# Performance work log

Hardware: AMD Instinct MI355X
Metric: run time of the kernel (lower is better)

Reference implementation:

```python
import jax, jax.numpy as jnp
import numpy as np

# DeepSeek-V3 MoE config (matches init_kwargs)
H = 1024          # hidden_size
I = 704           # moe_intermediate_size
E = 64            # n_routed_experts
TOP_K = 8         # num_experts_per_tok
NG = 8            # n_group
TOPK_GROUP = 4    # topk_group
N_SHARED = 2      # n_shared_experts
ROUTED_SCALE = 2.5
S_I = I * N_SHARED  # shared expert intermediate size


def setup_inputs() -> dict:
    key = jax.random.key(0)
    ks = jax.random.split(key, 10)
    sc = 0.02
    return {
        "hidden_states": jax.random.normal(ks[0], (1, 1024, H), dtype=jnp.float32),
        "gate_w": sc * jax.random.normal(ks[1], (E, H), dtype=jnp.float32),
        "gate_bias": sc * jax.random.normal(ks[2], (E,), dtype=jnp.float32),  # e_score_correction_bias
        "Wg": sc * jax.random.normal(ks[3], (E, I, H), dtype=jnp.float32),
        "Wu": sc * jax.random.normal(ks[4], (E, I, H), dtype=jnp.float32),
        "Wd": sc * jax.random.normal(ks[5], (E, H, I), dtype=jnp.float32),
        "Sg": sc * jax.random.normal(ks[6], (S_I, H), dtype=jnp.float32),
        "Su": sc * jax.random.normal(ks[7], (S_I, H), dtype=jnp.float32),
        "Sd": sc * jax.random.normal(ks[8], (H, S_I), dtype=jnp.float32),
    }


def _route(x, gate_w, gate_bias):
    # x: [T, H] -> dense routing weight matrix [T, E]
    T = x.shape[0]
    logits = x @ gate_w.T                         # [T, E] (fp32, as HF casts to float32)
    scores = jax.nn.sigmoid(logits)
    scores_for_choice = scores + gate_bias[None, :]
    # group scores: sum of top-2 expert scores in each group
    grp = scores_for_choice.reshape(T, NG, E // NG)
    group_scores = jnp.sum(jax.lax.top_k(grp, 2)[0], axis=-1)      # [T, NG]
    _, gidx = jax.lax.top_k(group_scores, TOPK_GROUP)              # [T, TOPK_GROUP]
    gmask = jnp.zeros((T, NG), dtype=scores.dtype).at[
        jnp.arange(T)[:, None], gidx].set(1.0)                      # [T, NG]
    emask = jnp.repeat(gmask, E // NG, axis=1)                      # [T, E]
    masked = jnp.where(emask > 0, scores_for_choice, 0.0)
    _, topk_idx = jax.lax.top_k(masked, TOP_K)                      # [T, TOP_K]
    topk_w = jnp.take_along_axis(scores, topk_idx, axis=1)          # gather from UNbiased scores
    topk_w = topk_w / (jnp.sum(topk_w, axis=-1, keepdims=True) + 1e-20)  # norm_topk_prob
    topk_w = topk_w * ROUTED_SCALE
    # dense [T, E] combine weights (zeros for unrouted experts)
    rw = jnp.zeros((T, E), dtype=scores.dtype).at[
        jnp.arange(T)[:, None], topk_idx].add(topk_w)
    return rw


def _mlp(x, gw, uw, dw):
    # SwiGLU MLP: down(silu(gate(x)) * up(x)), no biases
    return (jax.nn.silu(x @ gw.T) * (x @ uw.T)) @ dw.T


def reference(hidden_states, gate_w, gate_bias, Wg, Wu, Wd, Sg, Su, Sd):
    B, S, _ = hidden_states.shape
    x = hidden_states.reshape(B * S, H)                 # [T, H]
    rw = _route(x, gate_w, gate_bias)                   # [T, E]
    # dense reference: run every expert on every token, weighted combine
    expert_out = jax.vmap(lambda gw_, uw_, dw_: _mlp(x, gw_, uw_, dw_))(Wg, Wu, Wd)  # [E, T, H]
    routed = jnp.einsum('eth,te->th', expert_out, rw)   # [T, H]
    shared = _mlp(x, Sg, Su, Sd)                        # [T, H]
    out = (routed + shared).reshape(B, S, H)
    return out
```

## Files before the change

### kernel.cpp

```cpp
#include <hip/hip_runtime.h>
#include <hip/hip_bf16.h>
#include <cstdint>
#include <cstddef>

#define T_TOK 1024
#define H_DIM 1024
#define I_DIM 704
#define E_NUM 64
#define TOPK 8
#define NGRP 8
#define GSIZE 8
#define TOPKG 4
#define SI_DIM 1408
#define RSCALE 2.5f
#define NSLOT (T_TOK * TOPK)

#define AP 72

typedef short bf16x8 __attribute__((ext_vector_type(8)));
typedef float f32x4 __attribute__((ext_vector_type(4)));

__device__ inline unsigned pk2(float x, float y) {
    __hip_bfloat162 h2 = __float22bfloat162_rn(make_float2(x, y));
    unsigned u; __builtin_memcpy(&u, &h2, 4); return u;
}
__device__ inline unsigned short bf1(float x) {
    __hip_bfloat16 h = __float2bfloat16(x);
    unsigned short u; __builtin_memcpy(&u, &h, 2); return u;
}

__global__ __launch_bounds__(64) void route_kernel(
    const float* __restrict__ x, const float* __restrict__ gw, const float* __restrict__ gb,
    int* __restrict__ counts, int* __restrict__ tk_idx, float* __restrict__ tk_w)
{
    const int t = blockIdx.x;
    __shared__ float xs[H_DIM];
    __shared__ float raw[E_NUM];
    __shared__ float sc[E_NUM];
    __shared__ float masked[E_NUM];
    __shared__ float gsc[NGRP];
    const int tid = threadIdx.x;

    const float4* xrow = (const float4*)(x + (size_t)t * H_DIM);
    for (int i = tid; i < H_DIM / 4; i += 64) ((float4*)xs)[i] = xrow[i];
    __syncthreads();

    float a = 0.f;
    const float* w = gw + (size_t)tid * H_DIM;
    for (int h = 0; h < H_DIM; h += 4) {
        float4 w4 = *(const float4*)(w + h);
        a += xs[h] * w4.x + xs[h+1] * w4.y + xs[h+2] * w4.z + xs[h+3] * w4.w;
    }
    float s = 1.f / (1.f + expf(-a));
    raw[tid] = s;
    sc[tid] = s + gb[tid];
    __syncthreads();

    if (tid == 0) {
        for (int g = 0; g < NGRP; ++g) {
            float m1 = -1e30f, m2 = -1e30f;
            for (int j = 0; j < GSIZE; ++j) {
                float v = sc[g * GSIZE + j];
                if (v > m1) { m2 = m1; m1 = v; }
                else if (v > m2) { m2 = v; }
            }
            gsc[g] = m1 + m2;
        }
        bool gsel[NGRP];
        for (int g = 0; g < NGRP; ++g) gsel[g] = false;
        for (int k = 0; k < TOPKG; ++k) {
            int best = -1; float bv = -1e30f;
            for (int g = 0; g < NGRP; ++g)
                if (!gsel[g] && gsc[g] > bv) { bv = gsc[g]; best = g; }
            gsel[best] = true;
        }
        for (int e = 0; e < E_NUM; ++e)
            masked[e] = gsel[e / GSIZE] ? sc[e] : 0.0f;
        int idx[TOPK];
        float wsum = 0.f;
        for (int k = 0; k < TOPK; ++k) {
            int best = 0; float bv = -1e30f;
            for (int e = 0; e < E_NUM; ++e)
                if (masked[e] > bv) { bv = masked[e]; best = e; }
            masked[best] = -1e30f;
            idx[k] = best;
            wsum += raw[best];
        }
        float inv = RSCALE / (wsum + 1e-20f);
        for (int k = 0; k < TOPK; ++k) {
            tk_idx[t * TOPK + k] = idx[k];
            tk_w[t * TOPK + k] = raw[idx[k]] * inv;
            atomicAdd(&counts[idx[k]], 1);
        }
    }
}

__global__ void zero_kernel(int* counts, int* fillc)
{
    int i = threadIdx.x;
    if (i < E_NUM) { counts[i] = 0; fillc[i] = 0; }
}

__global__ void scan_kernel(const int* __restrict__ counts, int* __restrict__ offs)
{
    if (threadIdx.x == 0) {
        int acc = 0;
        for (int e = 0; e < E_NUM; ++e) { offs[e] = acc; acc += counts[e]; }
    }
}

__global__ void fill_kernel(const int* __restrict__ tk_idx, const float* __restrict__ tk_w,
                            const int* __restrict__ offs, int* __restrict__ fillc,
                            int* __restrict__ tok_list, float* __restrict__ w_list)
{
    int t = blockIdx.x * blockDim.x + threadIdx.x;
    if (t >= T_TOK) return;
    for (int k = 0; k < TOPK; ++k) {
        int e = tk_idx[t * TOPK + k];
        int pos = offs[e] + atomicAdd(&fillc[e], 1);
        tok_list[pos] = t;
        w_list[pos] = tk_w[t * TOPK + k];
    }
}

__global__ __launch_bounds__(256) void gateup_routed_mfma(
    const float* __restrict__ x, const float* __restrict__ Wg, const float* __restrict__ Wu,
    const int* __restrict__ offs, const int* __restrict__ counts,
    const int* __restrict__ tok_list, const float* __restrict__ w_list,
    unsigned short* __restrict__ act)
{
    const int e = blockIdx.z;
    const int cnt = counts[e];
    const int m0 = blockIdx.y * 128;
    if (m0 >= cnt) return;
    const int off = offs[e];
    const int n0 = blockIdx.x * 64;

    __shared__ unsigned short As[128 * AP];
    __shared__ unsigned short Bg[64 * AP];
    __shared__ unsigned short Bu[64 * AP];
    __shared__ int toks[128];
    __shared__ float wts[128];

    const int tid = threadIdx.x;
    if (tid < 128) {
        int s = m0 + tid;
        toks[tid] = (s < cnt) ? tok_list[off + s] : -1;
        wts[tid]  = (s < cnt) ? w_list[off + s] : 0.f;
    }
    __syncthreads();

    const int lane = tid & 63;
    const int wv = tid >> 6;
    const int lr = lane & 15;
    const int lq = lane >> 4;

    f32x4 accg[2][4], accu[2][4];
    #pragma unroll
    for (int i = 0; i < 2; ++i)
        #pragma unroll
        for (int j = 0; j < 4; ++j) {
            accg[i][j] = (f32x4){0.f, 0.f, 0.f, 0.f};
            accu[i][j] = (f32x4){0.f, 0.f, 0.f, 0.f};
        }

    const float* wgp = Wg + (size_t)e * I_DIM * H_DIM + (size_t)n0 * H_DIM;
    const float* wup = Wu + (size_t)e * I_DIM * H_DIM + (size_t)n0 * H_DIM;

    const int ar = tid >> 4;
    const int ac = (tid & 15) * 4;

    for (int k0 = 0; k0 < H_DIM; k0 += 64) {
        #pragma unroll
        for (int p = 0; p < 8; ++p) {
            int r = ar + p * 16;
            int tkn = toks[r];
            float4 v = make_float4(0.f, 0.f, 0.f, 0.f);
            if (tkn >= 0) v = *(const float4*)(x + (size_t)tkn * H_DIM + k0 + ac);
            *(uint2*)&As[r * AP + ac] = make_uint2(pk2(v.x, v.y), pk2(v.z, v.w));
        }
        #pragma unroll
        for (int p = 0; p < 4; ++p) {
            int r = ar + p * 16;
            float4 g = *(const float4*)(wgp + (size_t)r * H_DIM + k0 + ac);
            *(uint2*)&Bg[r * AP + ac] = make_uint2(pk2(g.x, g.y), pk2(g.z, g.w));
            float4 u = *(const float4*)(wup + (size_t)r * H_DIM + k0 + ac);
            *(uint2*)&Bu[r * AP + ac] = make_uint2(pk2(u.x, u.y), pk2(u.z, u.w));
        }
        __syncthreads();
        #pragma unroll
        for (int ks = 0; ks < 2; ++ks) {
            bf16x8 a0 = *(const bf16x8*)&As[(wv * 32 + lr) * AP + ks * 32 + lq * 8];
            bf16x8 a1 = *(const bf16x8*)&As[(wv * 32 + 16 + lr) * AP + ks * 32 + lq * 8];
            #pragma unroll
            for (int nj = 0; nj < 4; ++nj) {
                bf16x8 bg = *(const bf16x8*)&Bg[(nj * 16 + lr) * AP + ks * 32 + lq * 8];
                bf16x8 bu = *(const bf16x8*)&Bu[(nj * 16 + lr) * AP + ks * 32 + lq * 8];
                accg[0][nj] = __builtin_amdgcn_mfma_f32_16x16x32_bf16(a0, bg, accg[0][nj], 0, 0, 0);
                accg[1][nj] = __builtin_amdgcn_mfma_f32_16x16x32_bf16(a1, bg, accg[1][nj], 0, 0, 0);
                accu[0][nj] = __builtin_amdgcn_mfma_f32_16x16x32_bf16(a0, bu, accu[0][nj], 0, 0, 0);
                accu[1][nj] = __builtin_amdgcn_mfma_f32_16x16x32_bf16(a1, bu, accu[1][nj], 0, 0, 0);
            }
        }
        __syncthreads();
    }

    #pragma unroll
    for (int mi = 0; mi < 2; ++mi) {
        #pragma unroll
        for (int r = 0; r < 4; ++r) {
            int srow = wv * 32 + mi * 16 + lq * 4 + r;
            if (m0 + srow < cnt) {
                float w = wts[srow];
                unsigned short* ap = act + (size_t)(off + m0 + srow) * I_DIM + n0 + lr;
                #pragma unroll
                for (int nj = 0; nj < 4; ++nj) {
                    float g = accg[mi][nj][r];
                    float u = accu[mi][nj][r];
                    float a = w * (g / (1.f + __expf(-g))) * u;
                    ap[nj * 16] = bf1(a);
                }
            }
        }
    }
}

__global__ __launch_bounds__(256) void down_routed_mfma(
    const unsigned short* __restrict__ act, const float* __restrict__ Wd,
    const int* __restrict__ offs, const int* __restrict__ counts,
    const int* __restrict__ tok_list, float* __restrict__ out)
{
    const int e = blockIdx.z;
    const int cnt = counts[e];
    const int m0 = blockIdx.y * 128;
    if (m0 >= cnt) return;
    const int off = offs[e];
    const int n0 = blockIdx.x * 64;

    __shared__ unsigned short As[128 * AP];
    __shared__ unsigned short Bs[64 * AP];
    __shared__ int toks[128];

    const int tid = threadIdx.x;
    if (tid < 128) {
        int s = m0 + tid;
        toks[tid] = (s < cnt) ? tok_list[off + s] : 0;
    }
    __syncthreads();

    const int lane = tid & 63;
    const int wv = tid >> 6;
    const int lr = lane & 15;
    const int lq = lane >> 4;

    f32x4 acc[2][4];
    #pragma unroll
    for (int i = 0; i < 2; ++i)
        #pragma unroll
        for (int j = 0; j < 4; ++j)
            acc[i][j] = (f32x4){0.f, 0.f, 0.f, 0.f};

    const float* wdp = Wd + (size_t)e * H_DIM * I_DIM + (size_t)n0 * I_DIM;
    const unsigned short* ap0 = act + (size_t)(off + m0) * I_DIM;
    const int ar = tid >> 4;
    const int ac = (tid & 15) * 4;

    for (int k0 = 0; k0 < I_DIM; k0 += 64) {
        #pragma unroll
        for (int p = 0; p < 8; ++p) {
            int r = ar + p * 16;
            uint2 v = make_uint2(0u, 0u);
            if (m0 + r < cnt) v = *(const uint2*)(ap0 + (size_t)r * I_DIM + k0 + ac);
            *(uint2*)&As[r * AP + ac] = v;
        }
        #pragma unroll
        for (int p = 0; p < 4; ++p) {
            int r = ar + p * 16;
            float4 w4 = *(const float4*)(wdp + (size_t)r * I_DIM + k0 + ac);
            *(uint2*)&Bs[r * AP + ac] = make_uint2(pk2(w4.x, w4.y), pk2(w4.z, w4.w));
        }
        __syncthreads();
        #pragma unroll
        for (int ks = 0; ks < 2; ++ks) {
            bf16x8 a0 = *(const bf16x8*)&As[(wv * 32 + lr) * AP + ks * 32 + lq * 8];
            bf16x8 a1 = *(const bf16x8*)&As[(wv * 32 + 16 + lr) * AP + ks * 32 + lq * 8];
            #pragma unroll
            for (int nj = 0; nj < 4; ++nj) {
                bf16x8 b = *(const bf16x8*)&Bs[(nj * 16 + lr) * AP + ks * 32 + lq * 8];
                acc[0][nj] = __builtin_amdgcn_mfma_f32_16x16x32_bf16(a0, b, acc[0][nj], 0, 0, 0);
                acc[1][nj] = __builtin_amdgcn_mfma_f32_16x16x32_bf16(a1, b, acc[1][nj], 0, 0, 0);
            }
        }
        __syncthreads();
    }

    #pragma unroll
    for (int mi = 0; mi < 2; ++mi) {
        #pragma unroll
        for (int r = 0; r < 4; ++r) {
            int srow = wv * 32 + mi * 16 + lq * 4 + r;
            if (m0 + srow < cnt) {
                int t = toks[srow];
                float* op = out + (size_t)t * H_DIM + n0 + lr;
                #pragma unroll
                for (int nj = 0; nj < 4; ++nj)
                    atomicAdd(&op[nj * 16], acc[mi][nj][r]);
            }
        }
    }
}

__global__ __launch_bounds__(256) void gateup_shared_mfma(
    const float* __restrict__ x, const float* __restrict__ Sg, const float* __restrict__ Su,
    unsigned short* __restrict__ sact)
{
    const int m0 = blockIdx.y * 128;
    const int n0 = blockIdx.x * 64;

    __shared__ unsigned short As[128 * AP];
    __shared__ unsigned short Bg[64 * AP];
    __shared__ unsigned short Bu[64 * AP];

    const int tid = threadIdx.x;
    const int lane = tid & 63;
    const int wv = tid >> 6;
    const int lr = lane & 15;
    const int lq = lane >> 4;

    f32x4 accg[2][4], accu[2][4];
    #pragma unroll
    for (int i = 0; i < 2; ++i)
        #pragma unroll
        for (int j = 0; j < 4; ++j) {
            accg[i][j] = (f32x4){0.f, 0.f, 0.f, 0.f};
            accu[i][j] = (f32x4){0.f, 0.f, 0.f, 0.f};
        }

    const float* gp = Sg + (size_t)n0 * H_DIM;
    const float* up = Su + (size_t)n0 * H_DIM;
    const int ar = tid >> 4;
    const int ac = (tid & 15) * 4;

    for (int k0 = 0; k0 < H_DIM; k0 += 64) {
        #pragma unroll
        for (int p = 0; p < 8; ++p) {
            int r = ar + p * 16;
            float4 v = *(const float4*)(x + (size_t)(m0 + r) * H_DIM + k0 + ac);
            *(uint2*)&As[r * AP + ac] = make_uint2(pk2(v.x, v.y), pk2(v.z, v.w));
        }
        #pragma unroll
        for (int p = 0; p < 4; ++p) {
            int r = ar + p * 16;
            float4 g = *(const float4*)(gp + (size_t)r * H_DIM + k0 + ac);
            *(uint2*)&Bg[r * AP + ac] = make_uint2(pk2(g.x, g.y), pk2(g.z, g.w));
            float4 u = *(const float4*)(up + (size_t)r * H_DIM + k0 + ac);
            *(uint2*)&Bu[r * AP + ac] = make_uint2(pk2(u.x, u.y), pk2(u.z, u.w));
        }
        __syncthreads();
        #pragma unroll
        for (int ks = 0; ks < 2; ++ks) {
            bf16x8 a0 = *(const bf16x8*)&As[(wv * 32 + lr) * AP + ks * 32 + lq * 8];
            bf16x8 a1 = *(const bf16x8*)&As[(wv * 32 + 16 + lr) * AP + ks * 32 + lq * 8];
            #pragma unroll
            for (int nj = 0; nj < 4; ++nj) {
                bf16x8 bg = *(const bf16x8*)&Bg[(nj * 16 + lr) * AP + ks * 32 + lq * 8];
                bf16x8 bu = *(const bf16x8*)&Bu[(nj * 16 + lr) * AP + ks * 32 + lq * 8];
                accg[0][nj] = __builtin_amdgcn_mfma_f32_16x16x32_bf16(a0, bg, accg[0][nj], 0, 0, 0);
                accg[1][nj] = __builtin_amdgcn_mfma_f32_16x16x32_bf16(a1, bg, accg[1][nj], 0, 0, 0);
                accu[0][nj] = __builtin_amdgcn_mfma_f32_16x16x32_bf16(a0, bu, accu[0][nj], 0, 0, 0);
                accu[1][nj] = __builtin_amdgcn_mfma_f32_16x16x32_bf16(a1, bu, accu[1][nj], 0, 0, 0);
            }
        }
        __syncthreads();
    }

    #pragma unroll
    for (int mi = 0; mi < 2; ++mi) {
        #pragma unroll
        for (int r = 0; r < 4; ++r) {
            int trow = m0 + wv * 32 + mi * 16 + lq * 4 + r;
            unsigned short* sp = sact + (size_t)trow * SI_DIM + n0 + lr;
            #pragma unroll
            for (int nj = 0; nj < 4; ++nj) {
                float g = accg[mi][nj][r];
                float u = accu[mi][nj][r];
                float a = (g / (1.f + __expf(-g))) * u;
                sp[nj * 16] = bf1(a);
            }
        }
    }
}

__global__ __launch_bounds__(256) void down_shared_mfma(
    const unsigned short* __restrict__ sact, const float* __restrict__ Sd,
    float* __restrict__ out)
{
    const int m0 = blockIdx.y * 128;
    const int n0 = blockIdx.x * 64;

    __shared__ unsigned short As[128 * AP];
    __shared__ unsigned short Bs[64 * AP];

    const int tid = threadIdx.x;
    const int lane = tid & 63;
    const int wv = tid >> 6;
    const int lr = lane & 15;
    const int lq = lane >> 4;

    f32x4 acc[2][4];
    #pragma unroll
    for (int i = 0; i < 2; ++i)
        #pragma unroll
        for (int j = 0; j < 4; ++j)
            acc[i][j] = (f32x4){0.f, 0.f, 0.f, 0.f};

    const float* wp = Sd + (size_t)n0 * SI_DIM;
    const int ar = tid >> 4;
    const int ac = (tid & 15) * 4;

    for (int k0 = 0; k0 < SI_DIM; k0 += 64) {
        #pragma unroll
        for (int p = 0; p < 8; ++p) {
            int r = ar + p * 16;
            uint2 v = *(const uint2*)(sact + (size_t)(m0 + r) * SI_DIM + k0 + ac);
            *(uint2*)&As[r * AP + ac] = v;
        }
        #pragma unroll
        for (int p = 0; p < 4; ++p) {
            int r = ar + p * 16;
            float4 w4 = *(const float4*)(wp + (size_t)r * SI_DIM + k0 + ac);
            *(uint2*)&Bs[r * AP + ac] = make_uint2(pk2(w4.x, w4.y), pk2(w4.z, w4.w));
        }
        __syncthreads();
        #pragma unroll
        for (int ks = 0; ks < 2; ++ks) {
            bf16x8 a0 = *(const bf16x8*)&As[(wv * 32 + lr) * AP + ks * 32 + lq * 8];
            bf16x8 a1 = *(const bf16x8*)&As[(wv * 32 + 16 + lr) * AP + ks * 32 + lq * 8];
            #pragma unroll
            for (int nj = 0; nj < 4; ++nj) {
                bf16x8 b = *(const bf16x8*)&Bs[(nj * 16 + lr) * AP + ks * 32 + lq * 8];
                acc[0][nj] = __builtin_amdgcn_mfma_f32_16x16x32_bf16(a0, b, acc[0][nj], 0, 0, 0);
                acc[1][nj] = __builtin_amdgcn_mfma_f32_16x16x32_bf16(a1, b, acc[1][nj], 0, 0, 0);
            }
        }
        __syncthreads();
    }

    #pragma unroll
    for (int mi = 0; mi < 2; ++mi) {
        #pragma unroll
        for (int r = 0; r < 4; ++r) {
            int trow = m0 + wv * 32 + mi * 16 + lq * 4 + r;
            float* op = out + (size_t)trow * H_DIM + n0 + lr;
            #pragma unroll
            for (int nj = 0; nj < 4; ++nj)
                op[nj * 16] = acc[mi][nj][r];
        }
    }
}

extern "C" void kernel_launch(void* const* d_in, const int* in_sizes, int n_in,
                              void* d_out, int out_size, void* d_ws, size_t ws_size,
                              hipStream_t stream)
{
    const float* x  = (const float*)d_in[0];
    const float* gw = (const float*)d_in[1];
    const float* gb = (const float*)d_in[2];
    const float* Wg = (const float*)d_in[3];
    const float* Wu = (const float*)d_in[4];
    const float* Wd = (const float*)d_in[5];
    const float* Sg = (const float*)d_in[6];
    const float* Su = (const float*)d_in[7];
    const float* Sd = (const float*)d_in[8];
    float* out = (float*)d_out;

    unsigned short* act  = (unsigned short*)d_ws;
    unsigned short* sact = act + (size_t)NSLOT * I_DIM;
    int* counts   = (int*)(sact + (size_t)T_TOK * SI_DIM);
    int* fillc    = counts + 64;
    int* offs     = fillc + 64;
    int* tk_idx   = offs + 64;
    float* tk_w   = (float*)(tk_idx + NSLOT);
    int* tok_list = (int*)(tk_w + NSLOT);
    float* w_list = (float*)(tok_list + NSLOT);

    zero_kernel<<<1, 64, 0, stream>>>(counts, fillc);
    route_kernel<<<T_TOK, 64, 0, stream>>>(x, gw, gb, counts, tk_idx, tk_w);
    scan_kernel<<<1, 64, 0, stream>>>(counts, offs);
    fill_kernel<<<4, 256, 0, stream>>>(tk_idx, tk_w, offs, fillc, tok_list, w_list);

    gateup_routed_mfma<<<dim3(11, 8, 64), 256, 0, stream>>>(x, Wg, Wu, offs, counts, tok_list, w_list, act);
    gateup_shared_mfma<<<dim3(22, 8, 1), 256, 0, stream>>>(x, Sg, Su, sact);
    down_shared_mfma<<<dim3(16, 8, 1), 256, 0, stream>>>(sact, Sd, out);
    down_routed_mfma<<<dim3(16, 8, 64), 256, 0, stream>>>(act, Wd, offs, counts, tok_list, out);
}
```

Before: 843.7 us.

## Register-prefetch next K tile in all GEMMs and replace atomic scatter with combine kernel

Each of the four MFMA GEMM kernels now issues the global loads for the next 64-wide K tile into registers before running the MFMAs on the current LDS tile, then converts and stores them to LDS after a barrier. This hides global-load latency behind compute. The routed down projection also stops doing float atomicAdd into the output. It writes per-slot results to a new workspace buffer, and a separate combine kernel sums the eight slots per token using positions recorded by fill_kernel. This trades atomic contention for extra workspace traffic, about 32 MB of slot_out, plus one more launch. The result is also deterministic.

```diff
diff --git a/kernel.cpp b/kernel.cpp
--- a/kernel.cpp
+++ b/kernel.cpp
@@ -111,7 +111,8 @@
 
 __global__ void fill_kernel(const int* __restrict__ tk_idx, const float* __restrict__ tk_w,
                             const int* __restrict__ offs, int* __restrict__ fillc,
-                            int* __restrict__ tok_list, float* __restrict__ w_list)
+                            int* __restrict__ tok_list, float* __restrict__ w_list,
+                            int* __restrict__ tk_pos)
 {
     int t = blockIdx.x * blockDim.x + threadIdx.x;
     if (t >= T_TOK) return;
@@ -120,6 +121,7 @@
         int pos = offs[e] + atomicAdd(&fillc[e], 1);
         tok_list[pos] = t;
         w_list[pos] = tk_w[t * TOPK + k];
+        tk_pos[t * TOPK + k] = pos;
     }
 }
 
@@ -145,7 +147,7 @@
     const int tid = threadIdx.x;
     if (tid < 128) {
         int s = m0 + tid;
-        toks[tid] = (s < cnt) ? tok_list[off + s] : -1;
+        toks[tid] = (s < cnt) ? tok_list[off + s] : 0;
         wts[tid]  = (s < cnt) ? w_list[off + s] : 0.f;
     }
     __syncthreads();
@@ -154,6 +156,15 @@
     const int wv = tid >> 6;
     const int lr = lane & 15;
     const int lq = lane >> 4;
+    const int ar = tid >> 4;
+    const int ac = (tid & 15) * 4;
+
+    const float* ax[8];
+    #pragma unroll
+    for (int p = 0; p < 8; ++p)
+        ax[p] = x + (size_t)toks[ar + p * 16] * H_DIM + ac;
+    const float* wgp = Wg + (size_t)e * I_DIM * H_DIM + (size_t)(n0 + ar) * H_DIM + ac;
+    const float* wup = Wu + (size_t)e * I_DIM * H_DIM + (size_t)(n0 + ar) * H_DIM + ac;
 
     f32x4 accg[2][4], accu[2][4];
     #pragma unroll
@@ -164,30 +175,36 @@
             accu[i][j] = (f32x4){0.f, 0.f, 0.f, 0.f};
         }
 
-    const float* wgp = Wg + (size_t)e * I_DIM * H_DIM + (size_t)n0 * H_DIM;
-    const float* wup = Wu + (size_t)e * I_DIM * H_DIM + (size_t)n0 * H_DIM;
-
-    const int ar = tid >> 4;
-    const int ac = (tid & 15) * 4;
+    float4 pa[8], pbg[4], pbu[4];
+
+    #pragma unroll
+    for (int p = 0; p < 8; ++p) pa[p] = *(const float4*)(ax[p]);
+    #pragma unroll
+    for (int p = 0; p < 4; ++p) {
+        pbg[p] = *(const float4*)(wgp + (size_t)p * 16 * H_DIM);
+        pbu[p] = *(const float4*)(wup + (size_t)p * 16 * H_DIM);
+    }
+    #pragma unroll
+    for (int p = 0; p < 8; ++p)
+        *(uint2*)&As[(ar + p * 16) * AP + ac] = make_uint2(pk2(pa[p].x, pa[p].y), pk2(pa[p].z, pa[p].w));
+    #pragma unroll
+    for (int p = 0; p < 4; ++p) {
+        *(uint2*)&Bg[(ar + p * 16) * AP + ac] = make_uint2(pk2(pbg[p].x, pbg[p].y), pk2(pbg[p].z, pbg[p].w));
+        *(uint2*)&Bu[(ar + p * 16) * AP + ac] = make_uint2(pk2(pbu[p].x, pbu[p].y), pk2(pbu[p].z, pbu[p].w));
+    }
+    __syncthreads();
 
     for (int k0 = 0; k0 < H_DIM; k0 += 64) {
-        #pragma unroll
-        for (int p = 0; p < 8; ++p) {
-            int r = ar + p * 16;
-            int tkn = toks[r];
-            float4 v = make_float4(0.f, 0.f, 0.f, 0.f);
-            if (tkn >= 0) v = *(const float4*)(x + (size_t)tkn * H_DIM + k0 + ac);
-            *(uint2*)&As[r * AP + ac] = make_uint2(pk2(v.x, v.y), pk2(v.z, v.w));
-        }
-        #pragma unroll
-        for (int p = 0; p < 4; ++p) {
-            int r = ar + p * 16;
-            float4 g = *(const float4*)(wgp + (size_t)r * H_DIM + k0 + ac);
-            *(uint2*)&Bg[r * AP + ac] = make_uint2(pk2(g.x, g.y), pk2(g.z, g.w));
-            float4 u = *(const float4*)(wup + (size_t)r * H_DIM + k0 + ac);
-            *(uint2*)&Bu[r * AP + ac] = make_uint2(pk2(u.x, u.y), pk2(u.z, u.w));
-        }
-        __syncthreads();
+        const int kn = k0 + 64;
+        if (kn < H_DIM) {
+            #pragma unroll
+            for (int p = 0; p < 8; ++p) pa[p] = *(const float4*)(ax[p] + kn);
+            #pragma unroll
+            for (int p = 0; p < 4; ++p) {
+                pbg[p] = *(const float4*)(wgp + (size_t)p * 16 * H_DIM + kn);
+                pbu[p] = *(const float4*)(wup + (size_t)p * 16 * H_DIM + kn);
+            }
+        }
         #pragma unroll
         for (int ks = 0; ks < 2; ++ks) {
             bf16x8 a0 = *(const bf16x8*)&As[(wv * 32 + lr) * AP + ks * 32 + lq * 8];
@@ -201,6 +218,16 @@
                 accu[0][nj] = __builtin_amdgcn_mfma_f32_16x16x32_bf16(a0, bu, accu[0][nj], 0, 0, 0);
                 accu[1][nj] = __builtin_amdgcn_mfma_f32_16x16x32_bf16(a1, bu, accu[1][nj], 0, 0, 0);
             }
+        }
+        if (kn >= H_DIM) break;
+        __syncthreads();
+        #pragma unroll
+        for (int p = 0; p < 8; ++p)
+            *(uint2*)&As[(ar + p * 16) * AP + ac] = make_uint2(pk2(pa[p].x, pa[p].y), pk2(pa[p].z, pa[p].w));
+        #pragma unroll
+        for (int p = 0; p < 4; ++p) {
+            *(uint2*)&Bg[(ar + p * 16) * AP + ac] = make_uint2(pk2(pbg[p].x, pbg[p].y), pk2(pbg[p].z, pbg[p].w));
+            *(uint2*)&Bu[(ar + p * 16) * AP + ac] = make_uint2(pk2(pbu[p].x, pbu[p].y), pk2(pbu[p].z, pbu[p].w));
         }
         __syncthreads();
     }
@@ -228,7 +255,7 @@
 __global__ __launch_bounds__(256) void down_routed_mfma(
     const unsigned short* __restrict__ act, const float* __restrict__ Wd,
     const int* __restrict__ offs, const int* __restrict__ counts,
-    const int* __restrict__ tok_list, float* __restrict__ out)
+    float* __restrict__ slot_out)
 {
     const int e = blockIdx.z;
     const int cnt = counts[e];
@@ -239,93 +266,128 @@
 
     __shared__ unsigned short As[128 * AP];
     __shared__ unsigned short Bs[64 * AP];
-    __shared__ int toks[128];
-
-    const int tid = threadIdx.x;
-    if (tid < 128) {
-        int s = m0 + tid;
-        toks[tid] = (s < cnt) ? tok_list[off + s] : 0;
-    }
-    __syncthreads();
-
-    const int lane = tid & 63;
-    const int wv = tid >> 6;
-    const int lr = lane & 15;
-    const int lq = lane >> 4;
-
-    f32x4 acc[2][4];
-    #pragma unroll
-    for (int i = 0; i < 2; ++i)
-        #pragma unroll
-        for (int j = 0; j < 4; ++j)
-            acc[i][j] = (f32x4){0.f, 0.f, 0.f, 0.f};
-
-    const float* wdp = Wd + (size_t)e * H_DIM * I_DIM + (size_t)n0 * I_DIM;
-    const unsigned short* ap0 = act + (size_t)(off + m0) * I_DIM;
-    const int ar = tid >> 4;
-    const int ac = (tid & 15) * 4;
-
-    for (int k0 = 0; k0 < I_DIM; k0 += 64) {
-        #pragma unroll
-        for (int p = 0; p < 8; ++p) {
-            int r = ar + p * 16;
-            uint2 v = make_uint2(0u, 0u);
-            if (m0 + r < cnt) v = *(const uint2*)(ap0 + (size_t)r * I_DIM + k0 + ac);
-            *(uint2*)&As[r * AP + ac] = v;
-        }
-        #pragma unroll
-        for (int p = 0; p < 4; ++p) {
-            int r = ar + p * 16;
-            float4 w4 = *(const float4*)(wdp + (size_t)r * I_DIM + k0 + ac);
-            *(uint2*)&Bs[r * AP + ac] = make_uint2(pk2(w4.x, w4.y), pk2(w4.z, w4.w));
-        }
-        __syncthreads();
-        #pragma unroll
-        for (int ks = 0; ks < 2; ++ks) {
-            bf16x8 a0 = *(const bf16x8*)&As[(wv * 32 + lr) * AP + ks * 32 + lq * 8];
-            bf16x8 a1 = *(const bf16x8*)&As[(wv * 32 + 16 + lr) * AP + ks * 32 + lq * 8];
-            #pragma unroll
-            for (int nj = 0; nj < 4; ++nj) {
-                bf16x8 b = *(const bf16x8*)&Bs[(nj * 16 + lr) * AP + ks * 32 + lq * 8];
-                acc[0][nj] = __builtin_amdgcn_mfma_f32_16x16x32_bf16(a0, b, acc[0][nj], 0, 0, 0);
-                acc[1][nj] = __builtin_amdgcn_mfma_f32_16x16x32_bf16(a1, b, acc[1][nj], 0, 0, 0);
-            }
-        }
-        __syncthreads();
-    }
-
-    #pragma unroll
-    for (int mi = 0; mi < 2; ++mi) {
-        #pragma unroll
-        for (int r = 0; r < 4; ++r) {
-            int srow = wv * 32 + mi * 16 + lq * 4 + r;
-            if (m0 + srow < cnt) {
-                int t = toks[srow];
-                float* op = out + (size_t)t * H_DIM + n0 + lr;
-                #pragma unroll
-                for (int nj = 0; nj < 4; ++nj)
-                    atomicAdd(&op[nj * 16], acc[mi][nj][r]);
-            }
-        }
-    }
-}
-
-__global__ __launch_bounds__(256) void gateup_shared_mfma(
-    const float* __restrict__ x, const float* __restrict__ Sg, const float* __restrict__ Su,
-    unsigned short* __restrict__ sact)
-{
-    const int m0 = blockIdx.y * 128;
-    const int n0 = blockIdx.x * 64;
-
-    __shared__ unsigned short As[128 * AP];
-    __shared__ unsigned short Bg[64 * AP];
-    __shared__ unsigned short Bu[64 * AP];
 
     const int tid = threadIdx.x;
     const int lane = tid & 63;
     const int wv = tid >> 6;
     const int lr = lane & 15;
     const int lq = lane >> 4;
+    const int ar = tid >> 4;
+    const int ac = (tid & 15) * 4;
+
+    const unsigned short* ap8[8];
+    #pragma unroll
+    for (int p = 0; p < 8; ++p) {
+        int r = m0 + ar + p * 16;
+        if (r > cnt - 1) r = cnt - 1;
+        ap8[p] = act + (size_t)(off + r) * I_DIM + ac;
+    }
+    const float* wdp = Wd + (size_t)e * H_DIM * I_DIM + (size_t)(n0 + ar) * I_DIM + ac;
+
+    f32x4 acc[2][4];
+    #pragma unroll
+    for (int i = 0; i < 2; ++i)
+        #pragma unroll
+        for (int j = 0; j < 4; ++j)
+            acc[i][j] = (f32x4){0.f, 0.f, 0.f, 0.f};
+
+    uint2 pa[8]; float4 pb[4];
+
+    #pragma unroll
+    for (int p = 0; p < 8; ++p) pa[p] = *(const uint2*)(ap8[p]);
+    #pragma unroll
+    for (int p = 0; p < 4; ++p) pb[p] = *(const float4*)(wdp + (size_t)p * 16 * I_DIM);
+    #pragma unroll
+    for (int p = 0; p < 8; ++p) *(uint2*)&As[(ar + p * 16) * AP + ac] = pa[p];
+    #pragma unroll
+    for (int p = 0; p < 4; ++p)
+        *(uint2*)&Bs[(ar + p * 16) * AP + ac] = make_uint2(pk2(pb[p].x, pb[p].y), pk2(pb[p].z, pb[p].w));
+    __syncthreads();
+
+    for (int k0 = 0; k0 < I_DIM; k0 += 64) {
+        const int kn = k0 + 64;
+        if (kn < I_DIM) {
+            #pragma unroll
+            for (int p = 0; p < 8; ++p) pa[p] = *(const uint2*)(ap8[p] + kn);
+            #pragma unroll
+            for (int p = 0; p < 4; ++p) pb[p] = *(const float4*)(wdp + (size_t)p * 16 * I_DIM + kn);
+        }
+        #pragma unroll
+        for (int ks = 0; ks < 2; ++ks) {
+            bf16x8 a0 = *(const bf16x8*)&As[(wv * 32 + lr) * AP + ks * 32 + lq * 8];
+            bf16x8 a1 = *(const bf16x8*)&As[(wv * 32 + 16 + lr) * AP + ks * 32 + lq * 8];
+            #pragma unroll
+            for (int nj = 0; nj < 4; ++nj) {
+                bf16x8 b = *(const bf16x8*)&Bs[(nj * 16 + lr) * AP + ks * 32 + lq * 8];
+                acc[0][nj] = __builtin_amdgcn_mfma_f32_16x16x32_bf16(a0, b, acc[0][nj], 0, 0, 0);
+                acc[1][nj] = __builtin_amdgcn_mfma_f32_16x16x32_bf16(a1, b, acc[1][nj], 0, 0, 0);
+            }
+        }
+        if (kn >= I_DIM) break;
+        __syncthreads();
+        #pragma unroll
+        for (int p = 0; p < 8; ++p) *(uint2*)&As[(ar + p * 16) * AP + ac] = pa[p];
+        #pragma unroll
+        for (int p = 0; p < 4; ++p)
+            *(uint2*)&Bs[(ar + p * 16) * AP + ac] = make_uint2(pk2(pb[p].x, pb[p].y), pk2(pb[p].z, pb[p].w));
+        __syncthreads();
+    }
+
+    #pragma unroll
+    for (int mi = 0; mi < 2; ++mi) {
+        #pragma unroll
+        for (int r = 0; r < 4; ++r) {
+            int srow = wv * 32 + mi * 16 + lq * 4 + r;
+            if (m0 + srow < cnt) {
+                float* op = slot_out + (size_t)(off + m0 + srow) * H_DIM + n0 + lr;
+                #pragma unroll
+                for (int nj = 0; nj < 4; ++nj)
+                    op[nj * 16] = acc[mi][nj][r];
+            }
+        }
+    }
+}
+
+__global__ __launch_bounds__(256) void combine_kernel(
+    const float* __restrict__ slot_out, const int* __restrict__ tk_pos,
+    float* __restrict__ out)
+{
+    const int t = blockIdx.x;
+    __shared__ int pos[TOPK];
+    if (threadIdx.x < TOPK) pos[threadIdx.x] = tk_pos[t * TOPK + threadIdx.x];
+    __syncthreads();
+    const int i = threadIdx.x;
+    float4 a = ((const float4*)(out + (size_t)t * H_DIM))[i];
+    #pragma unroll
+    for (int k = 0; k < TOPK; ++k) {
+        float4 v = ((const float4*)(slot_out + (size_t)pos[k] * H_DIM))[i];
+        a.x += v.x; a.y += v.y; a.z += v.z; a.w += v.w;
+    }
+    ((float4*)(out + (size_t)t * H_DIM))[i] = a;
+}
+
+__global__ __launch_bounds__(256) void gateup_shared_mfma(
+    const float* __restrict__ x, const float* __restrict__ Sg, const float* __restrict__ Su,
+    unsigned short* __restrict__ sact)
+{
+    const int m0 = blockIdx.y * 128;
+    const int n0 = blockIdx.x * 64;
+
+    __shared__ unsigned short As[128 * AP];
+    __shared__ unsigned short Bg[64 * AP];
+    __shared__ unsigned short Bu[64 * AP];
+
+    const int tid = threadIdx.x;
+    const int lane = tid & 63;
+    const int wv = tid >> 6;
+    const int lr = lane & 15;
+    const int lq = lane >> 4;
+    const int ar = tid >> 4;
+    const int ac = (tid & 15) * 4;
+
+    const float* xp = x + (size_t)(m0 + ar) * H_DIM + ac;
+    const float* gp = Sg + (size_t)(n0 + ar) * H_DIM + ac;
+    const float* up = Su + (size_t)(n0 + ar) * H_DIM + ac;
 
     f32x4 accg[2][4], accu[2][4];
     #pragma unroll
@@ -336,27 +398,36 @@
             accu[i][j] = (f32x4){0.f, 0.f, 0.f, 0.f};
         }
 
-    const float* gp = Sg + (size_t)n0 * H_DIM;
-    const float* up = Su + (size_t)n0 * H_DIM;
-    const int ar = tid >> 4;
-    const int ac = (tid & 15) * 4;
+    float4 pa[8], pbg[4], pbu[4];
+
+    #pragma unroll
+    for (int p = 0; p < 8; ++p) pa[p] = *(const float4*)(xp + (size_t)p * 16 * H_DIM);
+    #pragma unroll
+    for (int p = 0; p < 4; ++p) {
+        pbg[p] = *(const float4*)(gp + (size_t)p * 16 * H_DIM);
+        pbu[p] = *(const float4*)(up + (size_t)p * 16 * H_DIM);
+    }
+    #pragma unroll
+    for (int p = 0; p < 8; ++p)
+        *(uint2*)&As[(ar + p * 16) * AP + ac] = make_uint2(pk2(pa[p].x, pa[p].y), pk2(pa[p].z, pa[p].w));
+    #pragma unroll
+    for (int p = 0; p < 4; ++p) {
+        *(uint2*)&Bg[(ar + p * 16) * AP + ac] = make_uint2(pk2(pbg[p].x, pbg[p].y), pk2(pbg[p].z, pbg[p].w));
+        *(uint2*)&Bu[(ar + p * 16) * AP + ac] = make_uint2(pk2(pbu[p].x, pbu[p].y), pk2(pbu[p].z, pbu[p].w));
+    }
+    __syncthreads();
 
     for (int k0 = 0; k0 < H_DIM; k0 += 64) {
-        #pragma unroll
-        for (int p = 0; p < 8; ++p) {
-            int r = ar + p * 16;
-            float4 v = *(const float4*)(x + (size_t)(m0 + r) * H_DIM + k0 + ac);
-            *(uint2*)&As[r * AP + ac] = make_uint2(pk2(v.x, v.y), pk2(v.z, v.w));
-        }
-        #pragma unroll
-        for (int p = 0; p < 4; ++p) {
-            int r = ar + p * 16;
-            float4 g = *(const float4*)(gp + (size_t)r * H_DIM + k0 + ac);
-            *(uint2*)&Bg[r * AP + ac] = make_uint2(pk2(g.x, g.y), pk2(g.z, g.w));
-            float4 u = *(const float4*)(up + (size_t)r * H_DIM + k0 + ac);
-            *(uint2*)&Bu[r * AP + ac] = make_uint2(pk2(u.x, u.y), pk2(u.z, u.w));
-        }
-        __syncthreads();
+        const int kn = k0 + 64;
+        if (kn < H_DIM) {
+            #pragma unroll
+            for (int p = 0; p < 8; ++p) pa[p] = *(const float4*)(xp + (size_t)p * 16 * H_DIM + kn);
+            #pragma unroll
+            for (int p = 0; p < 4; ++p) {
+                pbg[p] = *(const float4*)(gp + (size_t)p * 16 * H_DIM + kn);
+                pbu[p] = *(const float4*)(up + (size_t)p * 16 * H_DIM + kn);
+            }
+        }
         #pragma unroll
         for (int ks = 0; ks < 2; ++ks) {
             bf16x8 a0 = *(const bf16x8*)&As[(wv * 32 + lr) * AP + ks * 32 + lq * 8];
@@ -371,6 +442,16 @@
                 accu[1][nj] = __builtin_amdgcn_mfma_f32_16x16x32_bf16(a1, bu, accu[1][nj], 0, 0, 0);
             }
         }
+        if (kn >= H_DIM) break;
+        __syncthreads();
+        #pragma unroll
+        for (int p = 0; p < 8; ++p)
+            *(uint2*)&As[(ar + p * 16) * AP + ac] = make_uint2(pk2(pa[p].x, pa[p].y), pk2(pa[p].z, pa[p].w));
+        #pragma unroll
+        for (int p = 0; p < 4; ++p) {
+            *(uint2*)&Bg[(ar + p * 16) * AP + ac] = make_uint2(pk2(pbg[p].x, pbg[p].y), pk2(pbg[p].z, pbg[p].w));
+            *(uint2*)&Bu[(ar + p * 16) * AP + ac] = make_uint2(pk2(pbu[p].x, pbu[p].y), pk2(pbu[p].z, pbu[p].w));
+        }
         __syncthreads();
     }
 
@@ -406,6 +487,11 @@
     const int wv = tid >> 6;
     const int lr = lane & 15;
     const int lq = lane >> 4;
+    const int ar = tid >> 4;
+    const int ac = (tid & 15) * 4;
+
+    const unsigned short* sp = sact + (size_t)(m0 + ar) * SI_DIM + ac;
+    const float* wp = Sd + (size_t)(n0 + ar) * SI_DIM + ac;
 
     f32x4 acc[2][4];
     #pragma unroll
@@ -414,24 +500,27 @@
         for (int j = 0; j < 4; ++j)
             acc[i][j] = (f32x4){0.f, 0.f, 0.f, 0.f};
 
-    const float* wp = Sd + (size_t)n0 * SI_DIM;
-    const int ar = tid >> 4;
-    const int ac = (tid & 15) * 4;
+    uint2 pa[8]; float4 pb[4];
+
+    #pragma unroll
+    for (int p = 0; p < 8; ++p) pa[p] = *(const uint2*)(sp + (size_t)p * 16 * SI_DIM);
+    #pragma unroll
+    for (int p = 0; p < 4; ++p) pb[p] = *(const float4*)(wp + (size_t)p * 16 * SI_DIM);
+    #pragma unroll
+    for (int p = 0; p < 8; ++p) *(uint2*)&As[(ar + p * 16) * AP + ac] = pa[p];
+    #pragma unroll
+    for (int p = 0; p < 4; ++p)
+        *(uint2*)&Bs[(ar + p * 16) * AP + ac] = make_uint2(pk2(pb[p].x, pb[p].y), pk2(pb[p].z, pb[p].w));
+    __syncthreads();
 
     for (int k0 = 0; k0 < SI_DIM; k0 += 64) {
-        #pragma unroll
-        for (int p = 0; p < 8; ++p) {
-            int r = ar + p * 16;
-            uint2 v = *(const uint2*)(sact + (size_t)(m0 + r) * SI_DIM + k0 + ac);
-            *(uint2*)&As[r * AP + ac] = v;
-        }
-        #pragma unroll
-        for (int p = 0; p < 4; ++p) {
-            int r = ar + p * 16;
-            float4 w4 = *(const float4*)(wp + (size_t)r * SI_DIM + k0 + ac);
-            *(uint2*)&Bs[r * AP + ac] = make_uint2(pk2(w4.x, w4.y), pk2(w4.z, w4.w));
-        }
-        __syncthreads();
+        const int kn = k0 + 64;
+        if (kn < SI_DIM) {
+            #pragma unroll
+            for (int p = 0; p < 8; ++p) pa[p] = *(const uint2*)(sp + (size_t)p * 16 * SI_DIM + kn);
+            #pragma unroll
+            for (int p = 0; p < 4; ++p) pb[p] = *(const float4*)(wp + (size_t)p * 16 * SI_DIM + kn);
+        }
         #pragma unroll
         for (int ks = 0; ks < 2; ++ks) {
             bf16x8 a0 = *(const bf16x8*)&As[(wv * 32 + lr) * AP + ks * 32 + lq * 8];
@@ -443,6 +532,13 @@
                 acc[1][nj] = __builtin_amdgcn_mfma_f32_16x16x32_bf16(a1, b, acc[1][nj], 0, 0, 0);
             }
         }
+        if (kn >= SI_DIM) break;
+        __syncthreads();
+        #pragma unroll
+        for (int p = 0; p < 8; ++p) *(uint2*)&As[(ar + p * 16) * AP + ac] = pa[p];
+        #pragma unroll
+        for (int p = 0; p < 4; ++p)
+            *(uint2*)&Bs[(ar + p * 16) * AP + ac] = make_uint2(pk2(pb[p].x, pb[p].y), pk2(pb[p].z, pb[p].w));
         __syncthreads();
     }
 
@@ -474,7 +570,8 @@
     const float* Sd = (const float*)d_in[8];
     float* out = (float*)d_out;
 
-    unsigned short* act  = (unsigned short*)d_ws;
+    float* slot_out = (float*)d_ws;
+    unsigned short* act  = (unsigned short*)(slot_out + (size_t)NSLOT * H_DIM);
     unsigned short* sact = act + (size_t)NSLOT * I_DIM;
     int* counts   = (int*)(sact + (size_t)T_TOK * SI_DIM);
     int* fillc    = counts + 64;
@@ -483,14 +580,16 @@
     float* tk_w   = (float*)(tk_idx + NSLOT);
     int* tok_list = (int*)(tk_w + NSLOT);
     float* w_list = (float*)(tok_list + NSLOT);
+    int* tk_pos   = (int*)(w_list + NSLOT);
 
     zero_kernel<<<1, 64, 0, stream>>>(counts, fillc);
     route_kernel<<<T_TOK, 64, 0, stream>>>(x, gw, gb, counts, tk_idx, tk_w);
     scan_kernel<<<1, 64, 0, stream>>>(counts, offs);
-    fill_kernel<<<4, 256, 0, stream>>>(tk_idx, tk_w, offs, fillc, tok_list, w_list);
+    fill_kernel<<<4, 256, 0, stream>>>(tk_idx, tk_w, offs, fillc, tok_list, w_list, tk_pos);
 
     gateup_routed_mfma<<<dim3(11, 8, 64), 256, 0, stream>>>(x, Wg, Wu, offs, counts, tok_list, w_list, act);
     gateup_shared_mfma<<<dim3(22, 8, 1), 256, 0, stream>>>(x, Sg, Su, sact);
     down_shared_mfma<<<dim3(16, 8, 1), 256, 0, stream>>>(sact, Sd, out);
-    down_routed_mfma<<<dim3(16, 8, 64), 256, 0, stream>>>(act, Wd, offs, counts, tok_list, out);
-}
+    down_routed_mfma<<<dim3(16, 8, 64), 256, 0, stream>>>(act, Wd, offs, counts, slot_out);
+    combine_kernel<<<T_TOK, 256, 0, stream>>>(slot_out, tk_pos, out);
+}
```

Measured after the change: 860.4 us. No clear change (+2.0%).

## Restructure routed expert GEMMs with register-prefetched weights and deterministic slot combine

Applied to the files above, without the earlier changes.

Both routed expert kernels are rewritten so each wave streams its weight rows straight from global memory into registers as the MFMA A operand. The gathered token or activation tile goes into a double-buffered LDS tile that is prefetched one K-step ahead, which cuts per-step barriers and staging of weights. The routed down projection now writes per-slot fp32 rows instead of issuing float atomicAdds into the output. A new combine kernel sums the top-k slot rows per token using positions recorded in the fill kernel. This adds a large slot_out workspace and one extra kernel launch, and the gate/up tile narrows to 32 intermediate columns with gate and up split across waves and exchanged through LDS.

```diff
diff --git a/kernel.cpp b/kernel.cpp
--- a/kernel.cpp
+++ b/kernel.cpp
@@ -28,6 +28,13 @@
     __hip_bfloat16 h = __float2bfloat16(x);
     unsigned short u; __builtin_memcpy(&u, &h, 2); return u;
 }
+__device__ inline uint4 pkq(float4 a, float4 b) {
+    return make_uint4(pk2(a.x, a.y), pk2(a.z, a.w), pk2(b.x, b.y), pk2(b.z, b.w));
+}
+__device__ inline bf16x8 cvt8(float4 a, float4 b) {
+    unsigned u[4] = {pk2(a.x, a.y), pk2(a.z, a.w), pk2(b.x, b.y), pk2(b.z, b.w)};
+    bf16x8 r; __builtin_memcpy(&r, u, 16); return r;
+}
 
 __global__ __launch_bounds__(64) void route_kernel(
     const float* __restrict__ x, const float* __restrict__ gw, const float* __restrict__ gb,
@@ -111,7 +118,8 @@
 
 __global__ void fill_kernel(const int* __restrict__ tk_idx, const float* __restrict__ tk_w,
                             const int* __restrict__ offs, int* __restrict__ fillc,
-                            int* __restrict__ tok_list, float* __restrict__ w_list)
+                            int* __restrict__ tok_list, float* __restrict__ w_list,
+                            int* __restrict__ tk_pos)
 {
     int t = blockIdx.x * blockDim.x + threadIdx.x;
     if (t >= T_TOK) return;
@@ -120,10 +128,11 @@
         int pos = offs[e] + atomicAdd(&fillc[e], 1);
         tok_list[pos] = t;
         w_list[pos] = tk_w[t * TOPK + k];
-    }
-}
-
-__global__ __launch_bounds__(256) void gateup_routed_mfma(
+        tk_pos[t * TOPK + k] = pos;
+    }
+}
+
+__global__ __launch_bounds__(256, 4) void gateup_routed_mfma(
     const float* __restrict__ x, const float* __restrict__ Wg, const float* __restrict__ Wu,
     const int* __restrict__ offs, const int* __restrict__ counts,
     const int* __restrict__ tok_list, const float* __restrict__ w_list,
@@ -131,21 +140,19 @@
 {
     const int e = blockIdx.z;
     const int cnt = counts[e];
-    const int m0 = blockIdx.y * 128;
-    if (m0 >= cnt) return;
+    const int s0 = blockIdx.y * 128;
+    if (s0 >= cnt) return;
     const int off = offs[e];
-    const int n0 = blockIdx.x * 64;
-
-    __shared__ unsigned short As[128 * AP];
-    __shared__ unsigned short Bg[64 * AP];
-    __shared__ unsigned short Bu[64 * AP];
+    const int i0 = blockIdx.x * 32;
+
+    __shared__ unsigned short Bs[2][128 * AP];
     __shared__ int toks[128];
     __shared__ float wts[128];
 
     const int tid = threadIdx.x;
     if (tid < 128) {
-        int s = m0 + tid;
-        toks[tid] = (s < cnt) ? tok_list[off + s] : -1;
+        int s = s0 + tid;
+        toks[tid] = (s < cnt) ? tok_list[off + s] : 0;
         wts[tid]  = (s < cnt) ? w_list[off + s] : 0.f;
     }
     __syncthreads();
@@ -154,160 +161,193 @@
     const int wv = tid >> 6;
     const int lr = lane & 15;
     const int lq = lane >> 4;
-
-    f32x4 accg[2][4], accu[2][4];
-    #pragma unroll
-    for (int i = 0; i < 2; ++i)
-        #pragma unroll
-        for (int j = 0; j < 4; ++j) {
-            accg[i][j] = (f32x4){0.f, 0.f, 0.f, 0.f};
-            accu[i][j] = (f32x4){0.f, 0.f, 0.f, 0.f};
-        }
-
-    const float* wgp = Wg + (size_t)e * I_DIM * H_DIM + (size_t)n0 * H_DIM;
-    const float* wup = Wu + (size_t)e * I_DIM * H_DIM + (size_t)n0 * H_DIM;
-
-    const int ar = tid >> 4;
-    const int ac = (tid & 15) * 4;
-
+    const int rhalf = wv & 1;
+    const int isup = wv >> 1;
+
+    const float* wp = (isup ? Wu : Wg) + (size_t)e * I_DIM * H_DIM
+                    + (size_t)(i0 + rhalf * 16 + lr) * H_DIM + lq * 8;
+
+    const int trow = tid >> 1;
+    const int tc = (tid & 1) * 32;
+    const float* tp = x + (size_t)toks[trow] * H_DIM + tc;
+
+    f32x4 acc[8];
+    #pragma unroll
+    for (int j = 0; j < 8; ++j) acc[j] = (f32x4){0.f, 0.f, 0.f, 0.f};
+
+    float4 pw0, pw1, pw2, pw3;
+    float4 tf[8];
+
+    pw0 = *(const float4*)(wp + 0);
+    pw1 = *(const float4*)(wp + 4);
+    pw2 = *(const float4*)(wp + 32);
+    pw3 = *(const float4*)(wp + 36);
+    #pragma unroll
+    for (int j = 0; j < 8; ++j) tf[j] = *(const float4*)(tp + j * 4);
+    #pragma unroll
+    for (int c = 0; c < 4; ++c)
+        *(uint4*)&Bs[0][trow * AP + tc + c * 8] = pkq(tf[2*c], tf[2*c+1]);
+    __syncthreads();
+
+    int buf = 0;
     for (int k0 = 0; k0 < H_DIM; k0 += 64) {
-        #pragma unroll
-        for (int p = 0; p < 8; ++p) {
-            int r = ar + p * 16;
-            int tkn = toks[r];
-            float4 v = make_float4(0.f, 0.f, 0.f, 0.f);
-            if (tkn >= 0) v = *(const float4*)(x + (size_t)tkn * H_DIM + k0 + ac);
-            *(uint2*)&As[r * AP + ac] = make_uint2(pk2(v.x, v.y), pk2(v.z, v.w));
-        }
-        #pragma unroll
-        for (int p = 0; p < 4; ++p) {
-            int r = ar + p * 16;
-            float4 g = *(const float4*)(wgp + (size_t)r * H_DIM + k0 + ac);
-            *(uint2*)&Bg[r * AP + ac] = make_uint2(pk2(g.x, g.y), pk2(g.z, g.w));
-            float4 u = *(const float4*)(wup + (size_t)r * H_DIM + k0 + ac);
-            *(uint2*)&Bu[r * AP + ac] = make_uint2(pk2(u.x, u.y), pk2(u.z, u.w));
-        }
+        const int kn = k0 + 64;
+        bf16x8 af0 = cvt8(pw0, pw1);
+        bf16x8 af1 = cvt8(pw2, pw3);
+        if (kn < H_DIM) {
+            pw0 = *(const float4*)(wp + kn);
+            pw1 = *(const float4*)(wp + kn + 4);
+            pw2 = *(const float4*)(wp + kn + 32);
+            pw3 = *(const float4*)(wp + kn + 36);
+            #pragma unroll
+            for (int j = 0; j < 8; ++j) tf[j] = *(const float4*)(tp + kn + j * 4);
+        }
+        #pragma unroll
+        for (int ks = 0; ks < 2; ++ks) {
+            bf16x8 a = ks ? af1 : af0;
+            #pragma unroll
+            for (int nj = 0; nj < 8; ++nj) {
+                bf16x8 b = *(const bf16x8*)&Bs[buf][(nj * 16 + lr) * AP + ks * 32 + lq * 8];
+                acc[nj] = __builtin_amdgcn_mfma_f32_16x16x32_bf16(a, b, acc[nj], 0, 0, 0);
+            }
+        }
+        if (kn >= H_DIM) break;
+        #pragma unroll
+        for (int c = 0; c < 4; ++c)
+            *(uint4*)&Bs[buf ^ 1][trow * AP + tc + c * 8] = pkq(tf[2*c], tf[2*c+1]);
         __syncthreads();
-        #pragma unroll
-        for (int ks = 0; ks < 2; ++ks) {
-            bf16x8 a0 = *(const bf16x8*)&As[(wv * 32 + lr) * AP + ks * 32 + lq * 8];
-            bf16x8 a1 = *(const bf16x8*)&As[(wv * 32 + 16 + lr) * AP + ks * 32 + lq * 8];
-            #pragma unroll
-            for (int nj = 0; nj < 4; ++nj) {
-                bf16x8 bg = *(const bf16x8*)&Bg[(nj * 16 + lr) * AP + ks * 32 + lq * 8];
-                bf16x8 bu = *(const bf16x8*)&Bu[(nj * 16 + lr) * AP + ks * 32 + lq * 8];
-                accg[0][nj] = __builtin_amdgcn_mfma_f32_16x16x32_bf16(a0, bg, accg[0][nj], 0, 0, 0);
-                accg[1][nj] = __builtin_amdgcn_mfma_f32_16x16x32_bf16(a1, bg, accg[1][nj], 0, 0, 0);
-                accu[0][nj] = __builtin_amdgcn_mfma_f32_16x16x32_bf16(a0, bu, accu[0][nj], 0, 0, 0);
-                accu[1][nj] = __builtin_amdgcn_mfma_f32_16x16x32_bf16(a1, bu, accu[1][nj], 0, 0, 0);
-            }
-        }
-        __syncthreads();
-    }
-
-    #pragma unroll
-    for (int mi = 0; mi < 2; ++mi) {
-        #pragma unroll
-        for (int r = 0; r < 4; ++r) {
-            int srow = wv * 32 + mi * 16 + lq * 4 + r;
-            if (m0 + srow < cnt) {
-                float w = wts[srow];
-                unsigned short* ap = act + (size_t)(off + m0 + srow) * I_DIM + n0 + lr;
-                #pragma unroll
-                for (int nj = 0; nj < 4; ++nj) {
-                    float g = accg[mi][nj][r];
-                    float u = accu[mi][nj][r];
-                    float a = w * (g / (1.f + __expf(-g))) * u;
-                    ap[nj * 16] = bf1(a);
-                }
-            }
-        }
-    }
-}
-
-__global__ __launch_bounds__(256) void down_routed_mfma(
+        buf ^= 1;
+    }
+
+    __syncthreads();
+    float* gex = (float*)&Bs[0][0];
+    if (!isup) {
+        #pragma unroll
+        for (int nj = 0; nj < 8; ++nj)
+            *(f32x4*)&gex[((rhalf * 8 + nj) * 64 + lane) * 4] = acc[nj];
+    }
+    __syncthreads();
+    if (isup) {
+        #pragma unroll
+        for (int nj = 0; nj < 8; ++nj) {
+            int sl = nj * 16 + lr;
+            f32x4 g = *(const f32x4*)&gex[((rhalf * 8 + nj) * 64 + lane) * 4];
+            float w = wts[sl];
+            unsigned short o[4];
+            #pragma unroll
+            for (int r = 0; r < 4; ++r) {
+                float gg = g[r];
+                float a = w * (gg / (1.f + __expf(-gg))) * acc[nj][r];
+                o[r] = bf1(a);
+            }
+            if (s0 + sl < cnt) {
+                uint2 pkd = make_uint2((unsigned)o[0] | ((unsigned)o[1] << 16),
+                                       (unsigned)o[2] | ((unsigned)o[3] << 16));
+                *(uint2*)(act + (size_t)(off + s0 + sl) * I_DIM + i0 + rhalf * 16 + lq * 4) = pkd;
+            }
+        }
+    }
+}
+
+__global__ __launch_bounds__(256, 4) void down_routed_mfma(
     const unsigned short* __restrict__ act, const float* __restrict__ Wd,
     const int* __restrict__ offs, const int* __restrict__ counts,
-    const int* __restrict__ tok_list, float* __restrict__ out)
+    float* __restrict__ slot_out)
 {
     const int e = blockIdx.z;
     const int cnt = counts[e];
-    const int m0 = blockIdx.y * 128;
-    if (m0 >= cnt) return;
+    const int s0 = blockIdx.y * 128;
+    if (s0 >= cnt) return;
     const int off = offs[e];
-    const int n0 = blockIdx.x * 64;
-
-    __shared__ unsigned short As[128 * AP];
-    __shared__ unsigned short Bs[64 * AP];
-    __shared__ int toks[128];
+    const int h0 = blockIdx.x * 64;
+
+    __shared__ unsigned short Bs[2][128 * AP];
 
     const int tid = threadIdx.x;
-    if (tid < 128) {
-        int s = m0 + tid;
-        toks[tid] = (s < cnt) ? tok_list[off + s] : 0;
-    }
-    __syncthreads();
-
     const int lane = tid & 63;
     const int wv = tid >> 6;
     const int lr = lane & 15;
     const int lq = lane >> 4;
 
-    f32x4 acc[2][4];
-    #pragma unroll
-    for (int i = 0; i < 2; ++i)
+    const float* wp = Wd + (size_t)e * H_DIM * I_DIM
+                    + (size_t)(h0 + wv * 16 + lr) * I_DIM + lq * 8;
+
+    int srow = s0 + (tid >> 1);
+    if (srow > cnt - 1) srow = cnt - 1;
+    const unsigned short* ap = act + (size_t)(off + srow) * I_DIM + (tid & 1) * 32;
+
+    f32x4 acc[8];
+    #pragma unroll
+    for (int j = 0; j < 8; ++j) acc[j] = (f32x4){0.f, 0.f, 0.f, 0.f};
+
+    float4 pw0, pw1, pw2, pw3;
+    uint4 tf[4];
+
+    pw0 = *(const float4*)(wp + 0);
+    pw1 = *(const float4*)(wp + 4);
+    pw2 = *(const float4*)(wp + 32);
+    pw3 = *(const float4*)(wp + 36);
+    #pragma unroll
+    for (int j = 0; j < 4; ++j) tf[j] = *(const uint4*)(ap + j * 8);
+    #pragma unroll
+    for (int j = 0; j < 4; ++j)
+        *(uint4*)&Bs[0][(tid >> 1) * AP + (tid & 1) * 32 + j * 8] = tf[j];
+    __syncthreads();
+
+    int buf = 0;
+    for (int k0 = 0; k0 < I_DIM; k0 += 64) {
+        const int kn = k0 + 64;
+        bf16x8 af0 = cvt8(pw0, pw1);
+        bf16x8 af1 = cvt8(pw2, pw3);
+        if (kn < I_DIM) {
+            pw0 = *(const float4*)(wp + kn);
+            pw1 = *(const float4*)(wp + kn + 4);
+            pw2 = *(const float4*)(wp + kn + 32);
+            pw3 = *(const float4*)(wp + kn + 36);
+            #pragma unroll
+            for (int j = 0; j < 4; ++j) tf[j] = *(const uint4*)(ap + kn + j * 8);
+        }
+        #pragma unroll
+        for (int ks = 0; ks < 2; ++ks) {
+            bf16x8 a = ks ? af1 : af0;
+            #pragma unroll
+            for (int nj = 0; nj < 8; ++nj) {
+                bf16x8 b = *(const bf16x8*)&Bs[buf][(nj * 16 + lr) * AP + ks * 32 + lq * 8];
+                acc[nj] = __builtin_amdgcn_mfma_f32_16x16x32_bf16(a, b, acc[nj], 0, 0, 0);
+            }
+        }
+        if (kn >= I_DIM) break;
         #pragma unroll
         for (int j = 0; j < 4; ++j)
-            acc[i][j] = (f32x4){0.f, 0.f, 0.f, 0.f};
-
-    const float* wdp = Wd + (size_t)e * H_DIM * I_DIM + (size_t)n0 * I_DIM;
-    const unsigned short* ap0 = act + (size_t)(off + m0) * I_DIM;
-    const int ar = tid >> 4;
-    const int ac = (tid & 15) * 4;
-
-    for (int k0 = 0; k0 < I_DIM; k0 += 64) {
-        #pragma unroll
-        for (int p = 0; p < 8; ++p) {
-            int r = ar + p * 16;
-            uint2 v = make_uint2(0u, 0u);
-            if (m0 + r < cnt) v = *(const uint2*)(ap0 + (size_t)r * I_DIM + k0 + ac);
-            *(uint2*)&As[r * AP + ac] = v;
-        }
-        #pragma unroll
-        for (int p = 0; p < 4; ++p) {
-            int r = ar + p * 16;
-            float4 w4 = *(const float4*)(wdp + (size_t)r * I_DIM + k0 + ac);
-            *(uint2*)&Bs[r * AP + ac] = make_uint2(pk2(w4.x, w4.y), pk2(w4.z, w4.w));
-        }
+            *(uint4*)&Bs[buf ^ 1][(tid >> 1) * AP + (tid & 1) * 32 + j * 8] = tf[j];
         __syncthreads();
-        #pragma unroll
-        for (int ks = 0; ks < 2; ++ks) {
-            bf16x8 a0 = *(const bf16x8*)&As[(wv * 32 + lr) * AP + ks * 32 + lq * 8];
-            bf16x8 a1 = *(const bf16x8*)&As[(wv * 32 + 16 + lr) * AP + ks * 32 + lq * 8];
-            #pragma unroll
-            for (int nj = 0; nj < 4; ++nj) {
-                bf16x8 b = *(const bf16x8*)&Bs[(nj * 16 + lr) * AP + ks * 32 + lq * 8];
-                acc[0][nj] = __builtin_amdgcn_mfma_f32_16x16x32_bf16(a0, b, acc[0][nj], 0, 0, 0);
-                acc[1][nj] = __builtin_amdgcn_mfma_f32_16x16x32_bf16(a1, b, acc[1][nj], 0, 0, 0);
-            }
-        }
-        __syncthreads();
-    }
-
-    #pragma unroll
-    for (int mi = 0; mi < 2; ++mi) {
-        #pragma unroll
-        for (int r = 0; r < 4; ++r) {
-            int srow = wv * 32 + mi * 16 + lq * 4 + r;
-            if (m0 + srow < cnt) {
-                int t = toks[srow];
-                float* op = out + (size_t)t * H_DIM + n0 + lr;
-                #pragma unroll
-                for (int nj = 0; nj < 4; ++nj)
-                    atomicAdd(&op[nj * 16], acc[mi][nj][r]);
-            }
-        }
-    }
+        buf ^= 1;
+    }
+
+    #pragma unroll
+    for (int nj = 0; nj < 8; ++nj) {
+        int sl = nj * 16 + lr;
+        if (s0 + sl < cnt)
+            *(f32x4*)(slot_out + (size_t)(off + s0 + sl) * H_DIM + h0 + wv * 16 + lq * 4) = acc[nj];
+    }
+}
+
+__global__ __launch_bounds__(256) void combine_kernel(
+    const float* __restrict__ slot_out, const int* __restrict__ tk_pos,
+    float* __restrict__ out)
+{
+    const int t = blockIdx.x;
+    __shared__ int pos[TOPK];
+    if (threadIdx.x < TOPK) pos[threadIdx.x] = tk_pos[t * TOPK + threadIdx.x];
+    __syncthreads();
+    const int i = threadIdx.x;
+    float4 a = ((const float4*)(out + (size_t)t * H_DIM))[i];
+    #pragma unroll
+    for (int k = 0; k < TOPK; ++k) {
+        float4 v = ((const float4*)(slot_out + (size_t)pos[k] * H_DIM))[i];
+        a.x += v.x; a.y += v.y; a.z += v.z; a.w += v.w;
+    }
+    ((float4*)(out + (size_t)t * H_DIM))[i] = a;
 }
 
 __global__ __launch_bounds__(256) void gateup_shared_mfma(
@@ -474,7 +514,8 @@
     const float* Sd = (const float*)d_in[8];
     float* out = (float*)d_out;
 
-    unsigned short* act  = (unsigned short*)d_ws;
+    float* slot_out = (float*)d_ws;
+    unsigned short* act  = (unsigned short*)(slot_out + (size_t)NSLOT * H_DIM);
     unsigned short* sact = act + (size_t)NSLOT * I_DIM;
     int* counts   = (int*)(sact + (size_t)T_TOK * SI_DIM);
     int* fillc    = counts + 64;
@@ -483,14 +524,16 @@
     float* tk_w   = (float*)(tk_idx + NSLOT);
     int* tok_list = (int*)(tk_w + NSLOT);
     float* w_list = (float*)(tok_list + NSLOT);
+    int* tk_pos   = (int*)(w_list + NSLOT);
 
     zero_kernel<<<1, 64, 0, stream>>>(counts, fillc);
     route_kernel<<<T_TOK, 64, 0, stream>>>(x, gw, gb, counts, tk_idx, tk_w);
     scan_kernel<<<1, 64, 0, stream>>>(counts, offs);
-    fill_kernel<<<4, 256, 0, stream>>>(tk_idx, tk_w, offs, fillc, tok_list, w_list);
-
-    gateup_routed_mfma<<<dim3(11, 8, 64), 256, 0, stream>>>(x, Wg, Wu, offs, counts, tok_list, w_list, act);
+    fill_kernel<<<4, 256, 0, stream>>>(tk_idx, tk_w, offs, fillc, tok_list, w_list, tk_pos);
+
+    gateup_routed_mfma<<<dim3(22, 8, 64), 256, 0, stream>>>(x, Wg, Wu, offs, counts, tok_list, w_list, act);
     gateup_shared_mfma<<<dim3(22, 8, 1), 256, 0, stream>>>(x, Sg, Su, sact);
     down_shared_mfma<<<dim3(16, 8, 1), 256, 0, stream>>>(sact, Sd, out);
-    down_routed_mfma<<<dim3(16, 8, 64), 256, 0, stream>>>(act, Wd, offs, counts, tok_list, out);
-}
+    down_routed_mfma<<<dim3(16, 8, 64), 256, 0, stream>>>(act, Wd, offs, counts, slot_out);
+    combine_kernel<<<T_TOK, 256, 0, stream>>>(slot_out, tk_pos, out);
+}
```

Measured after the change: 996.2 us. 1.18x slower.
